# Performance work log

Hardware: AMD Instinct MI355X
Metric: run time of the kernel (lower is better)

The kernel has to match this reference:

```python
import jax, jax.numpy as jnp
import numpy as np

FEAT_DIM = 2048
K = 512
MU = 0.9
RHO_A = 0.99
DELTA = 1.0
ALPHA_P = 1.0
ALPHA_R = 0.5
TOPK = 3
B = 4096


def setup_inputs() -> dict:
    key = jax.random.key(0)
    k1, k2, k3 = jax.random.split(key, 3)
    z_t = jax.random.normal(k1, (B, FEAT_DIM), dtype=jnp.float32)
    g_t = jax.random.randint(k2, (B,), 0, 2, dtype=jnp.int32)
    prototypes = jax.random.normal(k3, (K, FEAT_DIM), dtype=jnp.float32) * 0.01
    proto_age = jnp.zeros((K,), dtype=jnp.float32)
    m_a = jnp.zeros((FEAT_DIM,), dtype=jnp.float32)
    return {"z_t": z_t, "g_t": g_t, "prototypes": prototypes,
            "proto_age": proto_age, "m_a": m_a}


def _update_prototypes(prototypes, proto_age, zs, g):
    # Sequential, order-sensitive EMA update (torch loop -> lax.scan).
    def step(carry, inp):
        protos, age = carry
        z, gi = inp  # z: (D,), gi: bool
        d = jnp.sum((protos - z[None, :]) ** 2, axis=1)  # (K,)
        k = jnp.argmin(d)
        new_row = jnp.where(gi, MU * protos[k] + (1.0 - MU) * z, protos[k])
        protos = protos.at[k].set(new_row)
        age = age.at[k].add(gi.astype(age.dtype))
        return (protos, age), None
    (protos, age), _ = jax.lax.scan(step, (prototypes, proto_age), (zs, g))
    return protos, age


def reference(z_t, g_t, prototypes, proto_age, m_a):
    g = g_t.astype(bool)
    zs = jax.lax.stop_gradient(z_t)  # updates are @torch.no_grad()

    # 3a: momentum prototype update over gated-normal frames (sequential)
    protos_new, age_new = _update_prototypes(prototypes, proto_age, zs, g)

    # 3c part 1: anomaly centroid from rejected frames (m_a_init starts False)
    anom = (~g).astype(zs.dtype)  # (B,)
    cnt = jnp.sum(anom)
    z_a = jnp.sum(zs * anom[:, None], axis=0) / jnp.maximum(cnt, 1.0)  # (D,)
    has_anom = cnt > 0
    m_a_new = jnp.where(has_anom, z_a, m_a)

    # 3b: pull loss — cdist + topk smallest + mean of prototypes + MSE
    # squared distances give identical topk indices to euclidean cdist
    d2 = (jnp.sum(z_t ** 2, axis=1, keepdims=True)
          - 2.0 * z_t @ protos_new.T
          + jnp.sum(protos_new ** 2, axis=1)[None, :])  # (B, K)
    _, idx = jax.lax.top_k(-d2, TOPK)  # (B, TOPK) nearest prototypes
    m_bar = jax.lax.stop_gradient(jnp.mean(protos_new[idx], axis=1))  # (B, D)
    L_pull = jnp.mean((z_t - m_bar) ** 2)

    # 3c part 2: push loss — hinge repulsion from anomaly centroid
    dist = jnp.sqrt(jnp.sum((z_t - jax.lax.stop_gradient(m_a_new)[None, :]) ** 2, axis=1))
    L_push = jnp.where(has_anom, jnp.mean(jax.nn.relu(DELTA - dist)), 0.0)

    return ALPHA_P * L_pull + ALPHA_R * L_push
```

## Files before the change

### kernel.cpp

```cpp
#include <hip/hip_runtime.h>
#include <math.h>

#define B_N 4096
#define D_F 2048
#define K_P 512
#define NGMAX 4096
#define MU 0.9f
#define OMU (1.0f - MU)
#define LOG2MU (-0.15200309344504997f)
#define FLTMAX 3.402823466e+38f
#define IMAX 0x7FFFFFFF
#define TILE 64
#define SDPITCH 513

#define SMEM_FLOATS (64 * SDPITCH + 64 * 65 + 64 + 512)
#define SMEM_INTS (512 + 16)
#define SMEM_BYTES ((SMEM_FLOATS + SMEM_INTS) * 4)

__device__ __forceinline__ bool argless(float v1, int i1, float v2, int i2) {
    return (v1 < v2) || (v1 == v2 && i1 < i2);
}

template <int CTRL>
__device__ __forceinline__ unsigned dppmin_u(unsigned v) {
    unsigned t = (unsigned)__builtin_amdgcn_update_dpp((int)v, (int)v, CTRL, 0xf, 0xf, false);
    return min(v, t);
}
__device__ __forceinline__ unsigned wave_min_u(unsigned v) {
    v = dppmin_u<0x111>(v);
    v = dppmin_u<0x112>(v);
    v = dppmin_u<0x114>(v);
    v = dppmin_u<0x118>(v);
    v = dppmin_u<0x142>(v);
    v = dppmin_u<0x143>(v);
    return (unsigned)__builtin_amdgcn_readlane((int)v, 63);
}

__global__ void k_prep(const int* __restrict__ g, int* __restrict__ gsteps,
                       int* __restrict__ scal) {
    __shared__ int s[1024];
    __shared__ int base;
    int tid = threadIdx.x;
    if (tid == 0) base = 0;
    __syncthreads();
    for (int c = 0; c < 4; ++c) {
        int i = c * 1024 + tid;
        int gi = (g[i] != 0) ? 1 : 0;
        s[tid] = gi;
        __syncthreads();
        for (int off = 1; off < 1024; off <<= 1) {
            int v = (tid >= off) ? s[tid - off] : 0;
            __syncthreads();
            s[tid] += v;
            __syncthreads();
        }
        int pos = base + s[tid] - 1;
        if (gi) gsteps[pos] = i;
        __syncthreads();
        if (tid == 1023) base += s[1023];
        __syncthreads();
    }
    if (tid == 0) { scal[0] = base; scal[1] = B_N - base; }
}

__global__ void k_rownorm(const float* __restrict__ src, float* __restrict__ dst, int nrows) {
    int row = blockIdx.x * 4 + (threadIdx.x >> 6);
    int lane = threadIdx.x & 63;
    if (row >= nrows) return;
    const float* p = src + (size_t)row * D_F;
    float acc = 0.f;
    for (int d0 = lane * 4; d0 < D_F; d0 += 256) {
        float4 v = *(const float4*)(p + d0);
        acc += v.x * v.x + v.y * v.y + v.z * v.z + v.w * v.w;
    }
    for (int off = 32; off; off >>= 1) acc += __shfl_xor(acc, off);
    if (lane == 0) dst[row] = acc;
}

__global__ void k_colsum(const float* __restrict__ Z, const int* __restrict__ g,
                         float* __restrict__ anom_part) {
    int d = blockIdx.x * 256 + threadIdx.x;
    int rc = blockIdx.y;
    float acc = 0.f;
    int r0 = rc * 128;
    for (int r = r0; r < r0 + 128; ++r) {
        if (g[r] == 0) acc += Z[(size_t)r * D_F + d];
    }
    anom_part[(size_t)rc * D_F + d] = acc;
}

__global__ void k_fin_ma(const float* __restrict__ anom_part, const float* __restrict__ ma_in,
                         const int* __restrict__ scal, float* __restrict__ m_a_used,
                         float* __restrict__ scal_f) {
    __shared__ float red[1024];
    int tid = threadIdx.x;
    int na = scal[1];
    float m2 = 0.f;
    for (int dd = tid; dd < D_F; dd += 1024) {
        float s = 0.f;
        for (int c = 0; c < 32; ++c) s += anom_part[(size_t)c * D_F + dd];
        float v = (na > 0) ? (s / (float)na) : ma_in[dd];
        m_a_used[dd] = v;
        m2 += v * v;
    }
    red[tid] = m2;
    __syncthreads();
    for (int off = 512; off; off >>= 1) {
        if (tid < off) red[tid] += red[tid + off];
        __syncthreads();
    }
    if (tid == 0) scal_f[0] = red[0];
}

template <int MODE>
__global__ void k_gemm(const float* __restrict__ Z, const float* __restrict__ P0,
                       const float* __restrict__ Pn, const int* __restrict__ gsteps,
                       const int* __restrict__ scal, float* __restrict__ Gram,
                       float* __restrict__ Dot, float* __restrict__ Dotf) {
    int ng = scal[0];
    int M = (MODE == 0) ? (ng + K_P) : B_N;
    int N = (MODE == 0) ? ng : K_P;
    int mb = blockIdx.y * 64, nb = blockIdx.x * 64;
    if (mb >= M || nb >= N) return;
    if (MODE == 0 && (mb + 64 <= ng) && (nb + 64 <= mb)) return;

    __shared__ float As[16][68];
    __shared__ float Bs[16][68];
    __shared__ const float* rowA[64];
    __shared__ const float* rowB[64];

    int tid = threadIdx.x;
    if (tid < 64) {
        int gm = mb + tid;
        const float* pa = nullptr;
        if (MODE == 0) {
            if (gm < ng) pa = Z + (size_t)gsteps[gm] * D_F;
            else if (gm < ng + K_P) pa = P0 + (size_t)(gm - ng) * D_F;
        } else {
            if (gm < B_N) pa = Z + (size_t)gm * D_F;
        }
        rowA[tid] = pa;
    } else if (tid < 128) {
        int t = tid - 64;
        int gn = nb + t;
        const float* pb = nullptr;
        if (MODE == 0) { if (gn < ng) pb = Z + (size_t)gsteps[gn] * D_F; }
        else { if (gn < K_P) pb = Pn + (size_t)gn * D_F; }
        rowB[t] = pb;
    }
    __syncthreads();

    int r = tid & 63, kq = tid >> 6;
    int tm = tid >> 4, tn = tid & 15;
    const float* pa = rowA[r];
    const float* pb = rowB[r];

    float acc[4][4] = {};
    for (int k0 = 0; k0 < D_F; k0 += 16) {
        float4 av = pa ? *(const float4*)(pa + k0 + kq * 4) : make_float4(0.f, 0.f, 0.f, 0.f);
        float4 bv = pb ? *(const float4*)(pb + k0 + kq * 4) : make_float4(0.f, 0.f, 0.f, 0.f);
        __syncthreads();
        As[kq * 4 + 0][r] = av.x; As[kq * 4 + 1][r] = av.y;
        As[kq * 4 + 2][r] = av.z; As[kq * 4 + 3][r] = av.w;
        Bs[kq * 4 + 0][r] = bv.x; Bs[kq * 4 + 1][r] = bv.y;
        Bs[kq * 4 + 2][r] = bv.z; Bs[kq * 4 + 3][r] = bv.w;
        __syncthreads();
#pragma unroll
        for (int kk = 0; kk < 16; ++kk) {
            float4 a = *(const float4*)&As[kk][tm * 4];
            float4 b = *(const float4*)&Bs[kk][tn * 4];
            float aa[4] = {a.x, a.y, a.z, a.w};
            float bb[4] = {b.x, b.y, b.z, b.w};
#pragma unroll
            for (int i = 0; i < 4; ++i)
#pragma unroll
                for (int j = 0; j < 4; ++j) acc[i][j] += aa[i] * bb[j];
        }
    }

#pragma unroll
    for (int i = 0; i < 4; ++i) {
        int gm = mb + tm * 4 + i;
        if (gm >= M) continue;
        float* crow;
        if (MODE == 0)
            crow = (gm < ng) ? (Gram + (size_t)gm * NGMAX) : (Dot + (size_t)(gm - ng) * NGMAX);
        else
            crow = Dotf + (size_t)gm * K_P;
#pragma unroll
        for (int j = 0; j < 4; ++j) {
            int gn = nb + tn * 4 + j;
            if (gn < N) crow[gn] = acc[i][j];
        }
    }
}

__global__ __launch_bounds__(512, 1)
void k_scan_tiled(const float* __restrict__ Gram, const float* __restrict__ Dot,
                  const float* __restrict__ pn2_0, const float* __restrict__ zn2,
                  const int* __restrict__ gsteps, const int* __restrict__ scal,
                  int* __restrict__ winlist, int* __restrict__ clist,
                  int* __restrict__ cnt_out) {
    extern __shared__ char smem_raw[];
    float* sdot = (float*)smem_raw;
    float* sgram = sdot + 64 * SDPITCH;
    float* szn2 = sgram + 64 * 65;
    float* sscale = szn2 + 64;
    int* rowcnt = (int*)(sscale + 512);
    int* listlen = rowcnt + 512;

    int tid = threadIdx.x;
    int lane = tid & 63;
    int wave = tid >> 6;
    int ng = scal[0];

    rowcnt[tid] = 0;
    if (tid < 8) listlen[tid] = 0;
    __syncthreads();

    float pn2r[8];
    unsigned idxp[8];
    if (wave == 0) {
#pragma unroll
        for (int r = 0; r < 8; ++r) {
            pn2r[r] = pn2_0[r * 64 + lane];
            idxp[r] = (unsigned)((r << 6) | lane);
        }
    }

    int ntiles = (ng + TILE - 1) / TILE;
    for (int T = 0; T < ntiles; ++T) {
        int j0 = T * TILE;
        int tlen = min(TILE, ng - j0);

        sscale[tid] = exp2f((float)rowcnt[tid] * LOG2MU);

        {
            const float* basep = Dot + (size_t)(wave * 64) * NGMAX + j0 + lane;
            float* sb = sdot + lane * SDPITCH + wave * 64;
            const float* ss = sscale + wave * 64;
#pragma unroll 16
            for (int rr = 0; rr < 64; ++rr) {
                sb[rr] = basep[(size_t)rr * NGMAX] * ss[rr];
            }
        }
        {
            int len = listlen[wave];
            const int* cl = clist + (size_t)wave * NGMAX;
            int i = 0;
            for (; i + 8 <= len; i += 8) {
                int a[8];
#pragma unroll
                for (int q = 0; q < 8; ++q) a[q] = cl[i + q];
                float gv[8];
#pragma unroll
                for (int q = 0; q < 8; ++q) {
                    int t = (a[q] >> 20) & 4095;
                    gv[q] = Gram[(size_t)t * NGMAX + j0 + lane];
                }
                float wq[8];
#pragma unroll
                for (int q = 0; q < 8; ++q) {
                    int row = a[q] & 511;
                    int gq = (a[q] >> 9) & 2047;
                    int c = rowcnt[row];
                    wq[q] = OMU * exp2f((float)(c - 1 - gq) * LOG2MU);
                }
#pragma unroll
                for (int q = 0; q < 8; ++q) {
                    int row = a[q] & 511;
                    sdot[lane * SDPITCH + row] += wq[q] * gv[q];
                }
            }
            for (; i < len; ++i) {
                int a = cl[i];
                int row = a & 511;
                int gq = (a >> 9) & 2047;
                int t = (a >> 20) & 4095;
                int c = rowcnt[row];
                float wqs = OMU * exp2f((float)(c - 1 - gq) * LOG2MU);
                float gv = Gram[(size_t)t * NGMAX + j0 + lane];
                sdot[lane * SDPITCH + row] += wqs * gv;
            }
        }
        {
            int t = tid >> 3, xo = (tid & 7) * 8;
            const float* src = Gram + (size_t)(j0 + t) * NGMAX + j0 + xo;
            float4 a = *(const float4*)(src);
            float4 b = *(const float4*)(src + 4);
            float* dst = sgram + t * 65 + xo;
            dst[0] = a.x; dst[1] = a.y; dst[2] = a.z; dst[3] = a.w;
            dst[4] = b.x; dst[5] = b.y; dst[6] = b.z; dst[7] = b.w;
        }
        if (tid < TILE) {
            szn2[tid] = (tid < tlen) ? zn2[gsteps[j0 + tid]] : 0.f;
        }
        __syncthreads();

        if (wave == 0) {
            float d8[8];
#pragma unroll
            for (int r = 0; r < 8; ++r) d8[r] = sdot[r * 64 + lane];
            float z2c = szn2[0];
            float gnc = sgram[1];
            int stw_reg = 0;
            int pend_addr = -1;
            float pend_old = 0.f, pend_g = 0.f;

            for (int jl = 0; jl < tlen; ++jl) {
                if (pend_addr >= 0) {
                    sdot[pend_addr] = MU * pend_old + OMU * pend_g;
                }
                float pv[8];
                float nz2 = 0.f, ngn = 0.f;
                const bool hn = (jl + 1 < tlen);
                int xr = jl + 2 + lane;
                float grmw = sgram[jl * 65 + (xr < 64 ? xr : 63)];
                if (hn) {
                    const float* cb = sdot + (jl + 1) * SDPITCH;
#pragma unroll
                    for (int r = 0; r < 8; ++r) pv[r] = cb[r * 64 + lane];
                    nz2 = szn2[jl + 1];
                    ngn = sgram[(jl + 1) * 65 + (jl + 2)];
                } else {
#pragma unroll
                    for (int r = 0; r < 8; ++r) pv[r] = 0.f;
                }

                unsigned kk[8];
#pragma unroll
                for (int r = 0; r < 8; ++r) {
                    float v = (pn2r[r] + z2c) - 2.f * d8[r];
                    kk[r] = (__float_as_uint(v) & 0xFFFFFE00u) | idxp[r];
                }
                unsigned a01 = min(kk[0], kk[1]), a23 = min(kk[2], kk[3]);
                unsigned a45 = min(kk[4], kk[5]), a67 = min(kk[6], kk[7]);
                unsigned km = wave_min_u(min(min(a01, a23), min(a45, a67)));
                int ks = (int)(km & 511u);
                int wlane = ks & 63, wr = ks >> 6;

                bool do_rmw = (xr < tlen);
                int rmw_addr = xr * SDPITCH + ks;
                float rmw_old = 0.f;
                if (do_rmw) rmw_old = sdot[rmw_addr];

                stw_reg = (lane == jl) ? ks : stw_reg;

                bool mine = (lane == wlane);
#pragma unroll
                for (int r = 0; r < 8; ++r) {
                    if (mine && r == wr) {
                        pn2r[r] = MU * MU * pn2r[r] + 2.f * MU * OMU * d8[r] + OMU * OMU * z2c;
                        pv[r] = MU * pv[r] + OMU * gnc;
                    }
                }

#pragma unroll
                for (int r = 0; r < 8; ++r) d8[r] = pv[r];
                z2c = nz2; gnc = ngn;

                pend_addr = do_rmw ? rmw_addr : -1;
                pend_old = rmw_old;
                pend_g = grmw;
            }
            if (pend_addr >= 0) {
                sdot[pend_addr] = MU * pend_old + OMU * pend_g;
            }

            int wj = stw_reg;
            bool valid = (lane < tlen);
            int myL = wj >> 6;
            int rank = 0, mrow = 0, lpos = 0, lcnt = 0;
            for (int i = 0; i < tlen; ++i) {
                int wi = __builtin_amdgcn_readlane(wj, i);
                if (valid && wi == wj) {
                    mrow++;
                    if (i < lane) rank++;
                }
                if (valid && (wi >> 6) == myL) {
                    lcnt++;
                    if (i < lane) lpos++;
                }
            }
            bool first = valid && (rank == 0);
            bool firstL = valid && (lpos == 0);
            int base = rowcnt[wj];
            int lbase = listlen[myL];
            if (valid) {
                int gq = base + rank;
                winlist[(size_t)wj * NGMAX + gq] = j0 + lane;
                clist[(size_t)myL * NGMAX + lbase + lpos] =
                    wj | (gq << 9) | ((j0 + lane) << 20);
            }
            if (first) rowcnt[wj] += mrow;
            if (firstL) listlen[myL] += lcnt;
        }
        __syncthreads();
    }

    cnt_out[tid] = rowcnt[tid];
}

__global__ void k_mat(const float* __restrict__ Z, const float* __restrict__ P0,
                      const int* __restrict__ gsteps, const int* __restrict__ winlist,
                      const int* __restrict__ cnt, float* __restrict__ Pn) {
    int k = blockIdx.x;
    int tid = threadIdx.x;
    int c = cnt[k];
    float bw = exp2f((float)c * LOG2MU);
    const float4* p0r = (const float4*)(P0 + (size_t)k * D_F);
    float4 a0 = p0r[tid], a1 = p0r[tid + 256];
    a0.x *= bw; a0.y *= bw; a0.z *= bw; a0.w *= bw;
    a1.x *= bw; a1.y *= bw; a1.z *= bw; a1.w *= bw;
    const int* wl = winlist + (size_t)k * NGMAX;
    float w = OMU;
    for (int q = c - 1; q >= 0; --q) {
        int t = wl[q];
        const float4* zr = (const float4*)(Z + (size_t)gsteps[t] * D_F);
        float4 z0 = zr[tid], z1 = zr[tid + 256];
        a0.x += w * z0.x; a0.y += w * z0.y; a0.z += w * z0.z; a0.w += w * z0.w;
        a1.x += w * z1.x; a1.y += w * z1.y; a1.z += w * z1.z; a1.w += w * z1.w;
        w *= MU;
    }
    float4* pnr = (float4*)(Pn + (size_t)k * D_F);
    pnr[tid] = a0;
    pnr[tid + 256] = a1;
}

__global__ void k_top3(const float* __restrict__ Dotf, const float* __restrict__ pn2f,
                       const float* __restrict__ Z, const float* __restrict__ Pn,
                       float* __restrict__ rowsum) {
    int row = blockIdx.x * 4 + (threadIdx.x >> 6);
    int lane = threadIdx.x & 63;
    float bv0 = FLTMAX, bv1 = FLTMAX, bv2 = FLTMAX;
    int bi0 = IMAX, bi1 = IMAX, bi2 = IMAX;
    for (int t = 0; t < 8; ++t) {
        int k = lane + 64 * t;
        float v = pn2f[k] - 2.f * Dotf[(size_t)row * K_P + k];
        if (argless(v, k, bv0, bi0)) {
            bv2 = bv1; bi2 = bi1; bv1 = bv0; bi1 = bi0; bv0 = v; bi0 = k;
        } else if (argless(v, k, bv1, bi1)) {
            bv2 = bv1; bi2 = bi1; bv1 = v; bi1 = k;
        } else if (argless(v, k, bv2, bi2)) {
            bv2 = v; bi2 = k;
        }
    }
    for (int off = 32; off; off >>= 1) {
        float a0 = bv0, a1 = bv1, a2 = bv2;
        int x0 = bi0, x1 = bi1, x2 = bi2;
        float b0 = __shfl_xor(bv0, off), b1 = __shfl_xor(bv1, off), b2 = __shfl_xor(bv2, off);
        int y0 = __shfl_xor(bi0, off), y1 = __shfl_xor(bi1, off), y2 = __shfl_xor(bi2, off);
        float nv[3]; int ni[3];
#pragma unroll
        for (int s = 0; s < 3; ++s) {
            bool ta = argless(a0, x0, b0, y0);
            nv[s] = ta ? a0 : b0;
            ni[s] = ta ? x0 : y0;
            if (ta) { a0 = a1; x0 = x1; a1 = a2; x1 = x2; a2 = FLTMAX; x2 = IMAX; }
            else    { b0 = b1; y0 = y1; b1 = b2; y1 = y2; b2 = FLTMAX; y2 = IMAX; }
        }
        bv0 = nv[0]; bv1 = nv[1]; bv2 = nv[2];
        bi0 = ni[0]; bi1 = ni[1]; bi2 = ni[2];
    }
    const float* pa = Pn + (size_t)bi0 * D_F;
    const float* pb = Pn + (size_t)bi1 * D_F;
    const float* pc = Pn + (size_t)bi2 * D_F;
    const float* zr = Z + (size_t)row * D_F;
    const float third = 1.f / 3.f;
    float acc = 0.f;
    for (int d0 = lane * 4; d0 < D_F; d0 += 256) {
        float4 z = *(const float4*)(zr + d0);
        float4 A = *(const float4*)(pa + d0);
        float4 Bv = *(const float4*)(pb + d0);
        float4 C = *(const float4*)(pc + d0);
        float m, df;
        m = (A.x + Bv.x + C.x) * third; df = z.x - m; acc += df * df;
        m = (A.y + Bv.y + C.y) * third; df = z.y - m; acc += df * df;
        m = (A.z + Bv.z + C.z) * third; df = z.z - m; acc += df * df;
        m = (A.w + Bv.w + C.w) * third; df = z.w - m; acc += df * df;
    }
    for (int off = 32; off; off >>= 1) acc += __shfl_xor(acc, off);
    if (lane == 0) rowsum[row] = acc;
}

__global__ void k_push(const float* __restrict__ Z, const float* __restrict__ m_a_used,
                       const float* __restrict__ zn2, const float* __restrict__ scal_f,
                       float* __restrict__ rowpush) {
    int row = blockIdx.x * 4 + (threadIdx.x >> 6);
    int lane = threadIdx.x & 63;
    const float* zr = Z + (size_t)row * D_F;
    float acc = 0.f;
    for (int d0 = lane * 4; d0 < D_F; d0 += 256) {
        float4 z = *(const float4*)(zr + d0);
        float4 m = *(const float4*)(m_a_used + d0);
        acc += z.x * m.x + z.y * m.y + z.z * m.z + z.w * m.w;
    }
    for (int off = 32; off; off >>= 1) acc += __shfl_xor(acc, off);
    if (lane == 0) {
        float d2 = zn2[row] - 2.f * acc + scal_f[0];
        float dist = sqrtf(fmaxf(d2, 0.f));
        rowpush[row] = fmaxf(1.f - dist, 0.f);
    }
}

__global__ void k_final(const float* __restrict__ rowsum, const float* __restrict__ rowpush,
                        const int* __restrict__ scal, float* __restrict__ out) {
    __shared__ float red[1024];
    int tid = threadIdx.x;
    float s = 0.f;
    for (int i = tid; i < B_N; i += 1024) s += rowsum[i];
    red[tid] = s;
    __syncthreads();
    for (int off = 512; off; off >>= 1) {
        if (tid < off) red[tid] += red[tid + off];
        __syncthreads();
    }
    float pull = red[0] / ((float)B_N * (float)D_F);
    __syncthreads();
    float p = 0.f;
    for (int i = tid; i < B_N; i += 1024) p += rowpush[i];
    red[tid] = p;
    __syncthreads();
    for (int off = 512; off; off >>= 1) {
        if (tid < off) red[tid] += red[tid + off];
        __syncthreads();
    }
    if (tid == 0) {
        float lpush = (scal[1] > 0) ? (red[0] / (float)B_N) : 0.f;
        out[0] = pull + 0.5f * lpush;
    }
}

extern "C" void kernel_launch(void* const* d_in, const int* in_sizes, int n_in,
                              void* d_out, int out_size, void* d_ws, size_t ws_size,
                              hipStream_t stream) {
    const float* Z = (const float*)d_in[0];
    const int* g = (const int*)d_in[1];
    const float* P0 = (const float*)d_in[2];
    const float* ma_in = (const float*)d_in[4];
    float* out = (float*)d_out;

    float* ws = (float*)d_ws;
    float* Gram = ws;
    float* Dotf = ws;
    float* Dot = ws + (size_t)NGMAX * NGMAX;
    float* Pn = Dot + (size_t)K_P * NGMAX;
    float* zn2 = Pn + (size_t)K_P * D_F;
    float* pn2_0 = zn2 + B_N;
    float* pn2f = pn2_0 + K_P;
    float* anom_part = pn2f + K_P;
    float* m_a_used = anom_part + 32 * D_F;
    float* rowsum = m_a_used + D_F;
    float* rowpush = rowsum + B_N;
    float* scal_f = rowpush + B_N;
    int* gsteps = (int*)(scal_f + 16);
    int* cnt = gsteps + B_N;
    int* scal = cnt + K_P;
    int* winlist = scal + 16;
    int* clist = winlist + (size_t)K_P * NGMAX;

    hipFuncSetAttribute((const void*)k_scan_tiled,
                        hipFuncAttributeMaxDynamicSharedMemorySize, SMEM_BYTES);

    k_prep<<<1, 1024, 0, stream>>>(g, gsteps, scal);
    k_rownorm<<<(B_N + 3) / 4, 256, 0, stream>>>(Z, zn2, B_N);
    k_rownorm<<<(K_P + 3) / 4, 256, 0, stream>>>(P0, pn2_0, K_P);
    k_colsum<<<dim3(D_F / 256, 32), 256, 0, stream>>>(Z, g, anom_part);
    k_fin_ma<<<1, 1024, 0, stream>>>(anom_part, ma_in, scal, m_a_used, scal_f);
    k_gemm<0><<<dim3(NGMAX / 64, (NGMAX + K_P) / 64), 256, 0, stream>>>(
        Z, P0, Pn, gsteps, scal, Gram, Dot, Dotf);
    k_scan_tiled<<<1, 512, SMEM_BYTES, stream>>>(Gram, Dot, pn2_0, zn2, gsteps, scal,
                                                 winlist, clist, cnt);
    k_mat<<<K_P, 256, 0, stream>>>(Z, P0, gsteps, winlist, cnt, Pn);
    k_rownorm<<<(K_P + 3) / 4, 256, 0, stream>>>(Pn, pn2f, K_P);
    k_gemm<1><<<dim3(K_P / 64, B_N / 64), 256, 0, stream>>>(
        Z, P0, Pn, gsteps, scal, Gram, Dot, Dotf);
    k_top3<<<B_N / 4, 256, 0, stream>>>(Dotf, pn2f, Z, Pn, rowsum);
    k_push<<<B_N / 4, 256, 0, stream>>>(Z, m_a_used, zn2, scal_f, rowpush);
    k_final<<<1, 1024, 0, stream>>>(rowsum, rowpush, scal, out);
}
```

Before: 2.257 ms.

## Replace FP32 SIMT GEMMs with split-bf16 MFMA GEMMs (hi/lo three-product)

Both GEMMs (the gated-frame Gram/prototype-dot matrix and the final Z·Pn^T) now use bf16 MFMA instructions. Each fp32 operand is split into a high and a low bf16 part, and three products (hh, hl, lh) are summed to keep accuracy close to fp32. New split kernels pre-convert Z and P0, and k_mat also writes split copies of Pn. The aim is to move the large O(B²D) Gram GEMM off scalar FMA onto the matrix cores, paid for with extra conversion passes, more memory traffic and slightly reduced precision that could change argmin ties in the sequential scan.

```diff
diff --git a/kernel.cpp b/kernel.cpp
--- a/kernel.cpp
+++ b/kernel.cpp
@@ -17,6 +17,9 @@
 #define SMEM_INTS (512 + 16)
 #define SMEM_BYTES ((SMEM_FLOATS + SMEM_INTS) * 4)
 
+typedef __attribute__((ext_vector_type(8))) short short8v;
+typedef __attribute__((ext_vector_type(4))) float float4v;
+
 __device__ __forceinline__ bool argless(float v1, int i1, float v2, int i2) {
     return (v1 < v2) || (v1 == v2 && i1 < i2);
 }
@@ -61,6 +64,42 @@
         __syncthreads();
     }
     if (tid == 0) { scal[0] = base; scal[1] = B_N - base; }
+}
+
+__global__ void k_split(const float* __restrict__ src, unsigned short* __restrict__ hi,
+                        unsigned short* __restrict__ lo, int n4) {
+    int i = blockIdx.x * 256 + threadIdx.x;
+    if (i >= n4) return;
+    float4 v = ((const float4*)src)[i];
+    float xs[4] = {v.x, v.y, v.z, v.w};
+    unsigned short h[4], l[4];
+#pragma unroll
+    for (int q = 0; q < 4; ++q) {
+        unsigned b = __float_as_uint(xs[q]);
+        unsigned hb = b & 0xFFFF0000u;
+        float lf = xs[q] - __uint_as_float(hb);
+        h[q] = (unsigned short)(hb >> 16);
+        l[q] = (unsigned short)(__float_as_uint(lf) >> 16);
+    }
+    ((ushort4*)hi)[i] = make_ushort4(h[0], h[1], h[2], h[3]);
+    ((ushort4*)lo)[i] = make_ushort4(l[0], l[1], l[2], l[3]);
+}
+
+__device__ __forceinline__ void split_store(unsigned short* __restrict__ hi,
+                                            unsigned short* __restrict__ lo,
+                                            size_t idx, float4 v) {
+    float xs[4] = {v.x, v.y, v.z, v.w};
+    unsigned short h[4], l[4];
+#pragma unroll
+    for (int q = 0; q < 4; ++q) {
+        unsigned b = __float_as_uint(xs[q]);
+        unsigned hb = b & 0xFFFF0000u;
+        float lf = xs[q] - __uint_as_float(hb);
+        h[q] = (unsigned short)(hb >> 16);
+        l[q] = (unsigned short)(__float_as_uint(lf) >> 16);
+    }
+    *(ushort4*)(hi + idx) = make_ushort4(h[0], h[1], h[2], h[3]);
+    *(ushort4*)(lo + idx) = make_ushort4(l[0], l[1], l[2], l[3]);
 }
 
 __global__ void k_rownorm(const float* __restrict__ src, float* __restrict__ dst, int nrows) {
@@ -113,10 +152,12 @@
 }
 
 template <int MODE>
-__global__ void k_gemm(const float* __restrict__ Z, const float* __restrict__ P0,
-                       const float* __restrict__ Pn, const int* __restrict__ gsteps,
-                       const int* __restrict__ scal, float* __restrict__ Gram,
-                       float* __restrict__ Dot, float* __restrict__ Dotf) {
+__global__ __launch_bounds__(256)
+void k_gemm_mfma(const unsigned short* __restrict__ Zhi, const unsigned short* __restrict__ Zlo,
+                 const unsigned short* __restrict__ P0hi, const unsigned short* __restrict__ P0lo,
+                 const unsigned short* __restrict__ Pnhi, const unsigned short* __restrict__ Pnlo,
+                 const int* __restrict__ gsteps, const int* __restrict__ scal,
+                 float* __restrict__ Gram, float* __restrict__ Dot, float* __restrict__ Dotf) {
     int ng = scal[0];
     int M = (MODE == 0) ? (ng + K_P) : B_N;
     int N = (MODE == 0) ? ng : K_P;
@@ -124,73 +165,128 @@
     if (mb >= M || nb >= N) return;
     if (MODE == 0 && (mb + 64 <= ng) && (nb + 64 <= mb)) return;
 
-    __shared__ float As[16][68];
-    __shared__ float Bs[16][68];
-    __shared__ const float* rowA[64];
-    __shared__ const float* rowB[64];
+    __shared__ __align__(16) unsigned short Ah[64][40];
+    __shared__ __align__(16) unsigned short Al[64][40];
+    __shared__ __align__(16) unsigned short Bh[64][40];
+    __shared__ __align__(16) unsigned short Bl[64][40];
+    __shared__ const unsigned short* rAh[64];
+    __shared__ const unsigned short* rAl[64];
+    __shared__ const unsigned short* rBh[64];
+    __shared__ const unsigned short* rBl[64];
 
     int tid = threadIdx.x;
     if (tid < 64) {
         int gm = mb + tid;
-        const float* pa = nullptr;
+        const unsigned short *ph = nullptr, *pl = nullptr;
         if (MODE == 0) {
-            if (gm < ng) pa = Z + (size_t)gsteps[gm] * D_F;
-            else if (gm < ng + K_P) pa = P0 + (size_t)(gm - ng) * D_F;
+            if (gm < ng) {
+                size_t o = (size_t)gsteps[gm] * D_F;
+                ph = Zhi + o; pl = Zlo + o;
+            } else if (gm < ng + K_P) {
+                size_t o = (size_t)(gm - ng) * D_F;
+                ph = P0hi + o; pl = P0lo + o;
+            }
         } else {
-            if (gm < B_N) pa = Z + (size_t)gm * D_F;
-        }
-        rowA[tid] = pa;
+            if (gm < B_N) {
+                size_t o = (size_t)gm * D_F;
+                ph = Zhi + o; pl = Zlo + o;
+            }
+        }
+        rAh[tid] = ph; rAl[tid] = pl;
     } else if (tid < 128) {
         int t = tid - 64;
         int gn = nb + t;
-        const float* pb = nullptr;
-        if (MODE == 0) { if (gn < ng) pb = Z + (size_t)gsteps[gn] * D_F; }
-        else { if (gn < K_P) pb = Pn + (size_t)gn * D_F; }
-        rowB[t] = pb;
+        const unsigned short *ph = nullptr, *pl = nullptr;
+        if (MODE == 0) {
+            if (gn < ng) {
+                size_t o = (size_t)gsteps[gn] * D_F;
+                ph = Zhi + o; pl = Zlo + o;
+            }
+        } else {
+            if (gn < K_P) {
+                size_t o = (size_t)gn * D_F;
+                ph = Pnhi + o; pl = Pnlo + o;
+            }
+        }
+        rBh[t] = ph; rBl[t] = pl;
     }
     __syncthreads();
 
-    int r = tid & 63, kq = tid >> 6;
-    int tm = tid >> 4, tn = tid & 15;
-    const float* pa = rowA[r];
-    const float* pb = rowB[r];
-
-    float acc[4][4] = {};
-    for (int k0 = 0; k0 < D_F; k0 += 16) {
-        float4 av = pa ? *(const float4*)(pa + k0 + kq * 4) : make_float4(0.f, 0.f, 0.f, 0.f);
-        float4 bv = pb ? *(const float4*)(pb + k0 + kq * 4) : make_float4(0.f, 0.f, 0.f, 0.f);
-        __syncthreads();
-        As[kq * 4 + 0][r] = av.x; As[kq * 4 + 1][r] = av.y;
-        As[kq * 4 + 2][r] = av.z; As[kq * 4 + 3][r] = av.w;
-        Bs[kq * 4 + 0][r] = bv.x; Bs[kq * 4 + 1][r] = bv.y;
-        Bs[kq * 4 + 2][r] = bv.z; Bs[kq * 4 + 3][r] = bv.w;
-        __syncthreads();
-#pragma unroll
-        for (int kk = 0; kk < 16; ++kk) {
-            float4 a = *(const float4*)&As[kk][tm * 4];
-            float4 b = *(const float4*)&Bs[kk][tn * 4];
-            float aa[4] = {a.x, a.y, a.z, a.w};
-            float bb[4] = {b.x, b.y, b.z, b.w};
-#pragma unroll
-            for (int i = 0; i < 4; ++i)
-#pragma unroll
-                for (int j = 0; j < 4; ++j) acc[i][j] += aa[i] * bb[j];
-        }
-    }
-
-#pragma unroll
-    for (int i = 0; i < 4; ++i) {
-        int gm = mb + tm * 4 + i;
-        if (gm >= M) continue;
-        float* crow;
-        if (MODE == 0)
-            crow = (gm < ng) ? (Gram + (size_t)gm * NGMAX) : (Dot + (size_t)(gm - ng) * NGMAX);
-        else
-            crow = Dotf + (size_t)gm * K_P;
-#pragma unroll
-        for (int j = 0; j < 4; ++j) {
-            int gn = nb + tn * 4 + j;
-            if (gn < N) crow[gn] = acc[i][j];
+    int lrow = tid >> 2, lk = (tid & 3) * 8;
+    const unsigned short* pah = rAh[lrow];
+    const unsigned short* pal = rAl[lrow];
+    const unsigned short* pbh = rBh[lrow];
+    const unsigned short* pbl = rBl[lrow];
+
+    int wave = tid >> 6, lane = tid & 63;
+    int wr = (wave >> 1) * 32, wc = (wave & 1) * 32;
+    int fr = lane & 15, kg = lane >> 4;
+
+    float4v acc00 = {0.f, 0.f, 0.f, 0.f}, acc01 = {0.f, 0.f, 0.f, 0.f};
+    float4v acc10 = {0.f, 0.f, 0.f, 0.f}, acc11 = {0.f, 0.f, 0.f, 0.f};
+    const int4 z4i = make_int4(0, 0, 0, 0);
+
+    for (int k0 = 0; k0 < D_F; k0 += 32) {
+        int4 vah = pah ? *(const int4*)(pah + k0 + lk) : z4i;
+        int4 val = pal ? *(const int4*)(pal + k0 + lk) : z4i;
+        int4 vbh = pbh ? *(const int4*)(pbh + k0 + lk) : z4i;
+        int4 vbl = pbl ? *(const int4*)(pbl + k0 + lk) : z4i;
+        __syncthreads();
+        *(int4*)&Ah[lrow][lk] = vah;
+        *(int4*)&Al[lrow][lk] = val;
+        *(int4*)&Bh[lrow][lk] = vbh;
+        *(int4*)&Bl[lrow][lk] = vbl;
+        __syncthreads();
+
+        short8v ah0 = *(const short8v*)&Ah[wr + fr][kg * 8];
+        short8v ah1 = *(const short8v*)&Ah[wr + 16 + fr][kg * 8];
+        short8v al0 = *(const short8v*)&Al[wr + fr][kg * 8];
+        short8v al1 = *(const short8v*)&Al[wr + 16 + fr][kg * 8];
+        short8v bh0 = *(const short8v*)&Bh[wc + fr][kg * 8];
+        short8v bh1 = *(const short8v*)&Bh[wc + 16 + fr][kg * 8];
+        short8v bl0 = *(const short8v*)&Bl[wc + fr][kg * 8];
+        short8v bl1 = *(const short8v*)&Bl[wc + 16 + fr][kg * 8];
+
+        acc00 = __builtin_amdgcn_mfma_f32_16x16x32_bf16(ah0, bh0, acc00, 0, 0, 0);
+        acc00 = __builtin_amdgcn_mfma_f32_16x16x32_bf16(ah0, bl0, acc00, 0, 0, 0);
+        acc00 = __builtin_amdgcn_mfma_f32_16x16x32_bf16(al0, bh0, acc00, 0, 0, 0);
+
+        acc01 = __builtin_amdgcn_mfma_f32_16x16x32_bf16(ah0, bh1, acc01, 0, 0, 0);
+        acc01 = __builtin_amdgcn_mfma_f32_16x16x32_bf16(ah0, bl1, acc01, 0, 0, 0);
+        acc01 = __builtin_amdgcn_mfma_f32_16x16x32_bf16(al0, bh1, acc01, 0, 0, 0);
+
+        acc10 = __builtin_amdgcn_mfma_f32_16x16x32_bf16(ah1, bh0, acc10, 0, 0, 0);
+        acc10 = __builtin_amdgcn_mfma_f32_16x16x32_bf16(ah1, bl0, acc10, 0, 0, 0);
+        acc10 = __builtin_amdgcn_mfma_f32_16x16x32_bf16(al1, bh0, acc10, 0, 0, 0);
+
+        acc11 = __builtin_amdgcn_mfma_f32_16x16x32_bf16(ah1, bh1, acc11, 0, 0, 0);
+        acc11 = __builtin_amdgcn_mfma_f32_16x16x32_bf16(ah1, bl1, acc11, 0, 0, 0);
+        acc11 = __builtin_amdgcn_mfma_f32_16x16x32_bf16(al1, bh1, acc11, 0, 0, 0);
+    }
+
+#pragma unroll
+    for (int fm = 0; fm < 2; ++fm) {
+#pragma unroll
+        for (int i = 0; i < 4; ++i) {
+            int grow = mb + wr + fm * 16 + kg * 4 + i;
+            if (grow >= M) continue;
+            float* crow;
+            if (MODE == 0)
+                crow = (grow < ng) ? (Gram + (size_t)grow * NGMAX)
+                                   : (Dot + (size_t)(grow - ng) * NGMAX);
+            else
+                crow = Dotf + (size_t)grow * K_P;
+#pragma unroll
+            for (int fn = 0; fn < 2; ++fn) {
+                int gcol = nb + wc + fn * 16 + fr;
+                if (gcol >= N) continue;
+                float v;
+                if (fm == 0 && fn == 0) v = acc00[i];
+                else if (fm == 0 && fn == 1) v = acc01[i];
+                else if (fm == 1 && fn == 0) v = acc10[i];
+                else v = acc11[i];
+                crow[gcol] = v;
+            }
         }
     }
 }
@@ -403,7 +499,8 @@
 
 __global__ void k_mat(const float* __restrict__ Z, const float* __restrict__ P0,
                       const int* __restrict__ gsteps, const int* __restrict__ winlist,
-                      const int* __restrict__ cnt, float* __restrict__ Pn) {
+                      const int* __restrict__ cnt, float* __restrict__ Pn,
+                      unsigned short* __restrict__ Pnhi, unsigned short* __restrict__ Pnlo) {
     int k = blockIdx.x;
     int tid = threadIdx.x;
     int c = cnt[k];
@@ -425,6 +522,8 @@
     float4* pnr = (float4*)(Pn + (size_t)k * D_F);
     pnr[tid] = a0;
     pnr[tid + 256] = a1;
+    split_store(Pnhi, Pnlo, (size_t)k * D_F + (size_t)tid * 4, a0);
+    split_store(Pnhi, Pnlo, (size_t)k * D_F + (size_t)(tid + 256) * 4, a1);
 }
 
 __global__ void k_top3(const float* __restrict__ Dotf, const float* __restrict__ pn2f,
@@ -558,23 +657,31 @@
     int* scal = cnt + K_P;
     int* winlist = scal + 16;
     int* clist = winlist + (size_t)K_P * NGMAX;
+    unsigned short* Zhi = (unsigned short*)(clist + 8 * NGMAX);
+    unsigned short* Zlo = Zhi + (size_t)B_N * D_F;
+    unsigned short* P0hi = Zlo + (size_t)B_N * D_F;
+    unsigned short* P0lo = P0hi + (size_t)K_P * D_F;
+    unsigned short* Pnhi = P0lo + (size_t)K_P * D_F;
+    unsigned short* Pnlo = Pnhi + (size_t)K_P * D_F;
 
     hipFuncSetAttribute((const void*)k_scan_tiled,
                         hipFuncAttributeMaxDynamicSharedMemorySize, SMEM_BYTES);
 
     k_prep<<<1, 1024, 0, stream>>>(g, gsteps, scal);
+    k_split<<<(B_N * D_F / 4 + 255) / 256, 256, 0, stream>>>(Z, Zhi, Zlo, B_N * D_F / 4);
+    k_split<<<(K_P * D_F / 4 + 255) / 256, 256, 0, stream>>>(P0, P0hi, P0lo, K_P * D_F / 4);
     k_rownorm<<<(B_N + 3) / 4, 256, 0, stream>>>(Z, zn2, B_N);
     k_rownorm<<<(K_P + 3) / 4, 256, 0, stream>>>(P0, pn2_0, K_P);
     k_colsum<<<dim3(D_F / 256, 32), 256, 0, stream>>>(Z, g, anom_part);
     k_fin_ma<<<1, 1024, 0, stream>>>(anom_part, ma_in, scal, m_a_used, scal_f);
-    k_gemm<0><<<dim3(NGMAX / 64, (NGMAX + K_P) / 64), 256, 0, stream>>>(
-        Z, P0, Pn, gsteps, scal, Gram, Dot, Dotf);
+    k_gemm_mfma<0><<<dim3(NGMAX / 64, (NGMAX + K_P) / 64), 256, 0, stream>>>(
+        Zhi, Zlo, P0hi, P0lo, Pnhi, Pnlo, gsteps, scal, Gram, Dot, Dotf);
     k_scan_tiled<<<1, 512, SMEM_BYTES, stream>>>(Gram, Dot, pn2_0, zn2, gsteps, scal,
                                                  winlist, clist, cnt);
-    k_mat<<<K_P, 256, 0, stream>>>(Z, P0, gsteps, winlist, cnt, Pn);
+    k_mat<<<K_P, 256, 0, stream>>>(Z, P0, gsteps, winlist, cnt, Pn, Pnhi, Pnlo);
     k_rownorm<<<(K_P + 3) / 4, 256, 0, stream>>>(Pn, pn2f, K_P);
-    k_gemm<1><<<dim3(K_P / 64, B_N / 64), 256, 0, stream>>>(
-        Z, P0, Pn, gsteps, scal, Gram, Dot, Dotf);
+    k_gemm_mfma<1><<<dim3(K_P / 64, B_N / 64), 256, 0, stream>>>(
+        Zhi, Zlo, P0hi, P0lo, Pnhi, Pnlo, gsteps, scal, Gram, Dot, Dotf);
     k_top3<<<B_N / 4, 256, 0, stream>>>(Dotf, pn2f, Z, Pn, rowsum);
     k_push<<<B_N / 4, 256, 0, stream>>>(Z, m_a_used, zn2, scal_f, rowpush);
     k_final<<<1, 1024, 0, stream>>>(rowsum, rowpush, scal, out);
```

After: 1.892 ms, median of 2. 16.2% less time.
